# Kernel tuning notes

Measured on AMD Instinct MI355X. Metric: run time of the kernel, lower is better.

Reference implementation:

```python
import jax, jax.numpy as jnp
import numpy as np

B, C, U, N = 8, 64, 3, 512


def setup_inputs() -> dict:
    key = jax.random.key(0)
    k1, k2, k3, k4 = jax.random.split(key, 4)
    x = jax.random.normal(k1, (B, C, U, N), dtype=jnp.float32)
    # nn.Linear weights [out, in], applied as x @ W.T over channel dim
    s = 1.0 / np.sqrt(C)
    Wq = jax.random.uniform(k2, (C, C), dtype=jnp.float32, minval=-s, maxval=s)
    Wk = jax.random.uniform(k3, (C, C), dtype=jnp.float32, minval=-s, maxval=s)
    Wv = jax.random.uniform(k4, (C, C), dtype=jnp.float32, minval=-s, maxval=s)
    return {"x": x, "Wq": Wq, "Wk": Wk, "Wv": Wv}


def reference(x, Wq, Wk, Wv):
    # VNLinear: Linear over channel dim (dim 1), no bias: out[b,d,u,n] = sum_c x[b,c,u,n] W[d,c]
    def vn_linear(t, W):
        return jnp.einsum('bcun,dc->bdun', t, W)

    q = vn_linear(x, Wq)
    k = vn_linear(x, Wk)
    v = vn_linear(x, Wv)
    scale = x.shape[1] ** (-0.5)  # in_channels^-0.5
    # contraction over tiny vector-neuron dim u=3
    attn_logits = jnp.einsum('bcui,bcuj->bcij', q, k) * scale  # [B,C,N,N]
    attn_weights = jax.nn.softmax(attn_logits, axis=-1)
    out = jnp.einsum('bcij,bcuj->bcui', attn_weights, v)  # [B,C,U,N]
    return x + out
```

## Files before the change

kernel.cpp:

```cpp
#include <hip/hip_runtime.h>

#define BB 8
#define CC 64
#define UU 3
#define NN 512
#define POS (UU * NN)
#define QKV_ELEMS (BB * CC * POS)
#define SCALE2 0.1803368801111793f

__global__ __launch_bounds__(256) void proj_kernel(
    const float* __restrict__ x,
    const float* __restrict__ Wq,
    const float* __restrict__ Wk,
    const float* __restrict__ Wv,
    float* __restrict__ ws)
{
    const int blk   = blockIdx.x;
    const int bd2   = blk / 6;
    const int chunk = blk % 6;
    const int b     = bd2 >> 5;
    const int d0    = (bd2 & 31) * 2;
    const int tid   = threadIdx.x;
    const int p     = chunk * 256 + tid;

    __shared__ float w[6][CC];
    if (tid < 128) {
        int r = tid >> 6, c = tid & 63;
        w[r][c]     = Wq[(d0 + r) * CC + c];
        w[2 + r][c] = Wk[(d0 + r) * CC + c];
        w[4 + r][c] = Wv[(d0 + r) * CC + c];
    }
    __syncthreads();

    const float* xb = x + (size_t)b * CC * POS + p;
    float q0 = 0.f, q1 = 0.f, k0 = 0.f, k1 = 0.f, v0 = 0.f, v1 = 0.f;
    #pragma unroll 8
    for (int c = 0; c < CC; ++c) {
        float xv = xb[c * POS];
        q0 = fmaf(xv, w[0][c], q0);
        q1 = fmaf(xv, w[1][c], q1);
        k0 = fmaf(xv, w[2][c], k0);
        k1 = fmaf(xv, w[3][c], k1);
        v0 = fmaf(xv, w[4][c], v0);
        v1 = fmaf(xv, w[5][c], v1);
    }

    float* qs = ws;
    float* ks = ws + QKV_ELEMS;
    float* vs = ws + 2 * QKV_ELEMS;
    size_t base = (size_t)(b * CC + d0) * POS + p;
    qs[base] = q0 * SCALE2;  qs[base + POS] = q1 * SCALE2;
    ks[base] = k0;           ks[base + POS] = k1;
    vs[base] = v0;           vs[base + POS] = v1;
}

__global__ __launch_bounds__(256) void attn_kernel(
    const float* __restrict__ x,
    const float* __restrict__ ws,
    float* __restrict__ out)
{
    const int bd  = blockIdx.x;
    const int tid = threadIdx.x;

    __shared__ __align__(16) float ks[UU][NN];
    __shared__ __align__(16) float vs[UU][NN];
    __shared__ float4 part[NN];

    const float* qsg = ws + (size_t)bd * POS;
    const float* ksg = ws + QKV_ELEMS     + (size_t)bd * POS;
    const float* vsg = ws + 2 * QKV_ELEMS + (size_t)bd * POS;

    float* ksf = &ks[0][0];
    float* vsf = &vs[0][0];
    for (int t = tid; t < POS; t += 256) {
        ksf[t] = ksg[t];
        vsf[t] = vsg[t];
    }
    __syncthreads();

    const int r = tid >> 1;
    const int h = tid & 1;

    float q0[4], q1[4], q2[4];
    #pragma unroll
    for (int m = 0; m < 4; ++m) {
        int i = r + m * 128;
        q0[m] = qsg[i];
        q1[m] = qsg[NN + i];
        q2[m] = qsg[2 * NN + i];
    }

    float l[4]  = {0.f, 0.f, 0.f, 0.f};
    float a0[4] = {0.f, 0.f, 0.f, 0.f};
    float a1[4] = {0.f, 0.f, 0.f, 0.f};
    float a2[4] = {0.f, 0.f, 0.f, 0.f};

    const float4* k0p = (const float4*)&ks[0][0] + h * 64;
    const float4* k1p = (const float4*)&ks[1][0] + h * 64;
    const float4* k2p = (const float4*)&ks[2][0] + h * 64;
    const float4* v0p = (const float4*)&vs[0][0] + h * 64;
    const float4* v1p = (const float4*)&vs[1][0] + h * 64;
    const float4* v2p = (const float4*)&vs[2][0] + h * 64;

    for (int t = 0; t < 64; ++t) {
        float4 k0 = k0p[t];
        float4 k1 = k1p[t];
        float4 k2 = k2p[t];
        float4 v0 = v0p[t];
        float4 v1 = v1p[t];
        float4 v2 = v2p[t];

        #pragma unroll
        for (int m = 0; m < 4; ++m) {
            float s0 = fmaf(q0[m], k0.x, fmaf(q1[m], k1.x, q2[m] * k2.x));
            float s1 = fmaf(q0[m], k0.y, fmaf(q1[m], k1.y, q2[m] * k2.y));
            float s2 = fmaf(q0[m], k0.z, fmaf(q1[m], k1.z, q2[m] * k2.z));
            float s3 = fmaf(q0[m], k0.w, fmaf(q1[m], k1.w, q2[m] * k2.w));

            float p0 = __builtin_amdgcn_exp2f(s0);
            float p1 = __builtin_amdgcn_exp2f(s1);
            float p2 = __builtin_amdgcn_exp2f(s2);
            float p3 = __builtin_amdgcn_exp2f(s3);

            l[m] += (p0 + p1) + (p2 + p3);
            a0[m] = fmaf(p0, v0.x, fmaf(p1, v0.y, fmaf(p2, v0.z, fmaf(p3, v0.w, a0[m]))));
            a1[m] = fmaf(p0, v1.x, fmaf(p1, v1.y, fmaf(p2, v1.z, fmaf(p3, v1.w, a1[m]))));
            a2[m] = fmaf(p0, v2.x, fmaf(p1, v2.y, fmaf(p2, v2.z, fmaf(p3, v2.w, a2[m]))));
        }
    }

    #pragma unroll
    for (int m = 0; m < 4; ++m) {
        l[m]  += __shfl_xor(l[m],  1);
        a0[m] += __shfl_xor(a0[m], 1);
        a1[m] += __shfl_xor(a1[m], 1);
        a2[m] += __shfl_xor(a2[m], 1);
    }
    if (h == 0) {
        #pragma unroll
        for (int m = 0; m < 4; ++m) {
            part[r + m * 128] = make_float4(a0[m], a1[m], a2[m], l[m]);
        }
    }
    __syncthreads();

    const float* xd = x   + (size_t)bd * POS;
    float*       od = out + (size_t)bd * POS;
    #pragma unroll
    for (int w = 0; w < 2; ++w) {
        int i = tid + w * 256;
        float4 P = part[i];
        float inv = 1.0f / P.w;
        od[i]          = xd[i]          + P.x * inv;
        od[NN + i]     = xd[NN + i]     + P.y * inv;
        od[2 * NN + i] = xd[2 * NN + i] + P.z * inv;
    }
}

__global__ __launch_bounds__(256) void vn_attn_fused(
    const float* __restrict__ x,
    const float* __restrict__ Wq,
    const float* __restrict__ Wk,
    const float* __restrict__ Wv,
    float* __restrict__ out)
{
    const int bd  = blockIdx.x;
    const int b   = bd / CC;
    const int d   = bd % CC;
    const int tid = threadIdx.x;

    __shared__ float wq[CC], wk[CC], wv[CC];
    __shared__ float qs[UU][NN];
    __shared__ float ks[UU][NN];
    __shared__ float vs[UU][NN];

    if (tid < CC) {
        wq[tid] = Wq[d * CC + tid];
        wk[tid] = Wk[d * CC + tid];
        wv[tid] = Wv[d * CC + tid];
    }
    __syncthreads();

    const float* xb = x + (size_t)b * CC * POS;
    for (int p = tid; p < POS; p += 256) {
        float qa = 0.f, ka = 0.f, va = 0.f;
        #pragma unroll 8
        for (int c = 0; c < CC; ++c) {
            float xv = xb[c * POS + p];
            qa = fmaf(xv, wq[c], qa);
            ka = fmaf(xv, wk[c], ka);
            va = fmaf(xv, wv[c], va);
        }
        int u = p >> 9, n = p & (NN - 1);
        qs[u][n] = qa * SCALE2;
        ks[u][n] = ka;
        vs[u][n] = va;
    }
    __syncthreads();

    for (int i = tid; i < NN; i += 256) {
        float q0 = qs[0][i], q1 = qs[1][i], q2 = qs[2][i];
        float l = 0.f, a0 = 0.f, a1 = 0.f, a2 = 0.f;
        for (int j = 0; j < NN; j += 4) {
            float4 k0 = *(const float4*)&ks[0][j];
            float4 k1 = *(const float4*)&ks[1][j];
            float4 k2 = *(const float4*)&ks[2][j];
            float4 v0 = *(const float4*)&vs[0][j];
            float4 v1 = *(const float4*)&vs[1][j];
            float4 v2 = *(const float4*)&vs[2][j];
            float s0 = fmaf(q0, k0.x, fmaf(q1, k1.x, q2 * k2.x));
            float s1 = fmaf(q0, k0.y, fmaf(q1, k1.y, q2 * k2.y));
            float s2 = fmaf(q0, k0.z, fmaf(q1, k1.z, q2 * k2.z));
            float s3 = fmaf(q0, k0.w, fmaf(q1, k1.w, q2 * k2.w));
            float p0 = __builtin_amdgcn_exp2f(s0);
            float p1 = __builtin_amdgcn_exp2f(s1);
            float p2 = __builtin_amdgcn_exp2f(s2);
            float p3 = __builtin_amdgcn_exp2f(s3);
            l += p0 + p1 + p2 + p3;
            a0 = fmaf(p0, v0.x, fmaf(p1, v0.y, fmaf(p2, v0.z, fmaf(p3, v0.w, a0))));
            a1 = fmaf(p0, v1.x, fmaf(p1, v1.y, fmaf(p2, v1.z, fmaf(p3, v1.w, a1))));
            a2 = fmaf(p0, v2.x, fmaf(p1, v2.y, fmaf(p2, v2.z, fmaf(p3, v2.w, a2))));
        }
        float inv = 1.0f / l;
        size_t obase = ((size_t)(b * CC + d) * UU) * NN + i;
        const float* xd = xb + (size_t)d * POS;
        out[obase]          = xd[i]          + a0 * inv;
        out[obase + NN]     = xd[NN + i]     + a1 * inv;
        out[obase + 2 * NN] = xd[2 * NN + i] + a2 * inv;
    }
}

extern "C" void kernel_launch(void* const* d_in, const int* in_sizes, int n_in,
                              void* d_out, int out_size, void* d_ws, size_t ws_size,
                              hipStream_t stream) {
    const float* x  = (const float*)d_in[0];
    const float* Wq = (const float*)d_in[1];
    const float* Wk = (const float*)d_in[2];
    const float* Wv = (const float*)d_in[3];
    float* out = (float*)d_out;

    if (ws_size >= (size_t)3 * QKV_ELEMS * sizeof(float)) {
        float* ws = (float*)d_ws;
        proj_kernel<<<dim3(BB * 32 * 6), dim3(256), 0, stream>>>(x, Wq, Wk, Wv, ws);
        attn_kernel<<<dim3(BB * CC), dim3(256), 0, stream>>>(x, ws, out);
    } else {
        vn_attn_fused<<<dim3(BB * CC), dim3(256), 0, stream>>>(x, Wq, Wk, Wv, out);
    }
}
```

Baseline: 107.1 us.

## Split attention rows across two blocks per channel with 4-way key split

The attention kernel now launches two blocks per (batch, channel), each handling half of the query rows. Within a block, four threads split the key range and reduce with two shuffle steps. The key loop starts at a staggered offset per lane group to spread LDS bank access. K/V staging into shared memory uses float4 loads. This doubles the block count, from 512 to 1024, to fill more CUs, at the cost of loading K/V into shared memory twice per channel.

```diff
diff --git a/kernel.cpp b/kernel.cpp
--- a/kernel.cpp
+++ b/kernel.cpp
@@ -59,32 +59,40 @@
     const float* __restrict__ ws,
     float* __restrict__ out)
 {
-    const int bd  = blockIdx.x;
-    const int tid = threadIdx.x;
+    const int blk  = blockIdx.x;
+    const int bd   = blk >> 1;
+    const int half = blk & 1;
+    const int tid  = threadIdx.x;
 
     __shared__ __align__(16) float ks[UU][NN];
     __shared__ __align__(16) float vs[UU][NN];
-    __shared__ float4 part[NN];
+    __shared__ float4 part[NN / 2];
 
     const float* qsg = ws + (size_t)bd * POS;
     const float* ksg = ws + QKV_ELEMS     + (size_t)bd * POS;
     const float* vsg = ws + 2 * QKV_ELEMS + (size_t)bd * POS;
 
-    float* ksf = &ks[0][0];
-    float* vsf = &vs[0][0];
-    for (int t = tid; t < POS; t += 256) {
-        ksf[t] = ksg[t];
-        vsf[t] = vsg[t];
-    }
-    __syncthreads();
-
-    const int r = tid >> 1;
-    const int h = tid & 1;
+    {
+        const float4* kg4 = (const float4*)ksg;
+        const float4* vg4 = (const float4*)vsg;
+        float4* ks4 = (float4*)&ks[0][0];
+        float4* vs4 = (float4*)&vs[0][0];
+        #pragma unroll
+        for (int it = 0; it < 3; ++it) {
+            int idx = tid + it * 256;
+            if (idx < 384) ks4[idx] = kg4[idx];
+            else           vs4[idx - 384] = vg4[idx - 384];
+        }
+    }
+    __syncthreads();
+
+    const int h    = tid & 3;
+    const int slot = tid >> 2;
 
     float q0[4], q1[4], q2[4];
     #pragma unroll
     for (int m = 0; m < 4; ++m) {
-        int i = r + m * 128;
+        int i = half * 256 + slot + m * 64;
         q0[m] = qsg[i];
         q1[m] = qsg[NN + i];
         q2[m] = qsg[2 * NN + i];
@@ -95,14 +103,17 @@
     float a1[4] = {0.f, 0.f, 0.f, 0.f};
     float a2[4] = {0.f, 0.f, 0.f, 0.f};
 
-    const float4* k0p = (const float4*)&ks[0][0] + h * 64;
-    const float4* k1p = (const float4*)&ks[1][0] + h * 64;
-    const float4* k2p = (const float4*)&ks[2][0] + h * 64;
-    const float4* v0p = (const float4*)&vs[0][0] + h * 64;
-    const float4* v1p = (const float4*)&vs[1][0] + h * 64;
-    const float4* v2p = (const float4*)&vs[2][0] + h * 64;
-
-    for (int t = 0; t < 64; ++t) {
+    const float4* k0p = (const float4*)&ks[0][0] + h * 32;
+    const float4* k1p = (const float4*)&ks[1][0] + h * 32;
+    const float4* k2p = (const float4*)&ks[2][0] + h * 32;
+    const float4* v0p = (const float4*)&vs[0][0] + h * 32;
+    const float4* v1p = (const float4*)&vs[1][0] + h * 32;
+    const float4* v2p = (const float4*)&vs[2][0] + h * 32;
+    const int t0 = 2 * h;
+
+    #pragma unroll 2
+    for (int tt = 0; tt < 32; ++tt) {
+        const int t = (tt + t0) & 31;
         float4 k0 = k0p[t];
         float4 k1 = k1p[t];
         float4 k2 = k2p[t];
@@ -131,30 +142,27 @@
 
     #pragma unroll
     for (int m = 0; m < 4; ++m) {
-        l[m]  += __shfl_xor(l[m],  1);
-        a0[m] += __shfl_xor(a0[m], 1);
-        a1[m] += __shfl_xor(a1[m], 1);
-        a2[m] += __shfl_xor(a2[m], 1);
+        l[m]  += __shfl_xor(l[m],  1);  l[m]  += __shfl_xor(l[m],  2);
+        a0[m] += __shfl_xor(a0[m], 1);  a0[m] += __shfl_xor(a0[m], 2);
+        a1[m] += __shfl_xor(a1[m], 1);  a1[m] += __shfl_xor(a1[m], 2);
+        a2[m] += __shfl_xor(a2[m], 1);  a2[m] += __shfl_xor(a2[m], 2);
     }
     if (h == 0) {
         #pragma unroll
         for (int m = 0; m < 4; ++m) {
-            part[r + m * 128] = make_float4(a0[m], a1[m], a2[m], l[m]);
-        }
-    }
-    __syncthreads();
-
+            part[slot + m * 64] = make_float4(a0[m], a1[m], a2[m], l[m]);
+        }
+    }
+    __syncthreads();
+
+    const int i = half * 256 + tid;
+    float4 P = part[tid];
+    float inv = 1.0f / P.w;
     const float* xd = x   + (size_t)bd * POS;
     float*       od = out + (size_t)bd * POS;
-    #pragma unroll
-    for (int w = 0; w < 2; ++w) {
-        int i = tid + w * 256;
-        float4 P = part[i];
-        float inv = 1.0f / P.w;
-        od[i]          = xd[i]          + P.x * inv;
-        od[NN + i]     = xd[NN + i]     + P.y * inv;
-        od[2 * NN + i] = xd[2 * NN + i] + P.z * inv;
-    }
+    od[i]          = xd[i]          + P.x * inv;
+    od[NN + i]     = xd[NN + i]     + P.y * inv;
+    od[2 * NN + i] = xd[2 * NN + i] + P.z * inv;
 }
 
 __global__ __launch_bounds__(256) void vn_attn_fused(
@@ -242,7 +250,7 @@
     if (ws_size >= (size_t)3 * QKV_ELEMS * sizeof(float)) {
         float* ws = (float*)d_ws;
         proj_kernel<<<dim3(BB * 32 * 6), dim3(256), 0, stream>>>(x, Wq, Wk, Wv, ws);
-        attn_kernel<<<dim3(BB * CC), dim3(256), 0, stream>>>(x, ws, out);
+        attn_kernel<<<dim3(BB * CC * 2), dim3(256), 0, stream>>>(x, ws, out);
     } else {
         vn_attn_fused<<<dim3(BB * CC), dim3(256), 0, stream>>>(x, Wq, Wk, Wv, out);
     }
```

New measurement: 105.3 us. No clear change (-1.7%).
